# Kernel tuning notes

Hardware: AMD Instinct MI355X
Metric: run time of the kernel (lower is better)

The kernel has to match this reference:

```python
import jax, jax.numpy as jnp
import numpy as np

B, L, SD, PD, H, HD, OH = 2, 256, 64, 32, 4, 16, 32
EXP = 64  # MBConv hidden = pair_dim * expand_ratio(2)
SE = 16   # squeezed channels = int(64 * 0.25)


def _ln(x, g, b, eps=1e-5):
    m = jnp.mean(x, -1, keepdims=True)
    v = jnp.mean((x - m) ** 2, -1, keepdims=True)
    return (x - m) / jnp.sqrt(v + eps) * g + b


def _inorm(x, eps=1e-5):  # InstanceNorm2d (no affine), x: [B,C,H,W]
    m = jnp.mean(x, (2, 3), keepdims=True)
    v = jnp.mean((x - m) ** 2, (2, 3), keepdims=True)
    return (x - m) / jnp.sqrt(v + eps)


def setup_inputs() -> dict:
    key = jax.random.key(0)
    ks = jax.random.split(key, 16)
    s = jnp.float32(0.02)
    return dict(
        seq_repr=jax.random.normal(ks[0], (B, L, SD), jnp.float32),
        pair_repr=jax.random.normal(ks[1], (B, L, L, PD), jnp.float32),
        g_attn=jnp.ones((SD,), jnp.float32), b_attn=jnp.zeros((SD,), jnp.float32),
        g_pair=jnp.ones((PD,), jnp.float32), b_pair=jnp.zeros((PD,), jnp.float32),
        W_opm_lin=jax.random.normal(ks[2], (SD, OH), jnp.float32) * s,
        b_opm_lin=jnp.zeros((OH,), jnp.float32),
        g_opm=jnp.ones((OH * OH,), jnp.float32), b_opm=jnp.zeros((OH * OH,), jnp.float32),
        W_opm_proj=jax.random.normal(ks[3], (OH * OH, PD), jnp.float32) * s,
        b_opm_proj=jnp.zeros((PD,), jnp.float32),
        W_exp=jax.random.normal(ks[4], (EXP, PD), jnp.float32) * s,
        W_dw=jax.random.normal(ks[5], (EXP, 1, 3, 3), jnp.float32) * s,
        W_se1=jax.random.normal(ks[6], (SE, EXP), jnp.float32) * s,
        b_se1=jnp.zeros((SE,), jnp.float32),
        W_se2=jax.random.normal(ks[7], (EXP, SE), jnp.float32) * s,
        b_se2=jnp.zeros((EXP,), jnp.float32),
        W_pw=jax.random.normal(ks[8], (PD, EXP), jnp.float32) * s,
        W_qkv=jax.random.normal(ks[9], (SD, 3 * SD), jnp.float32) * s,
        W_outp=jax.random.normal(ks[10], (SD, SD), jnp.float32) * s,
        b_outp=jnp.zeros((SD,), jnp.float32),
        W_bias=jax.random.normal(ks[11], (PD, H), jnp.float32) * s,
    )


def reference(seq_repr, pair_repr, g_attn, b_attn, g_pair, b_pair,
              W_opm_lin, b_opm_lin, g_opm, b_opm, W_opm_proj, b_opm_proj,
              W_exp, W_dw, W_se1, b_se1, W_se2, b_se2, W_pw,
              W_qkv, W_outp, b_outp, W_bias):
    # --- OuterProductMean on attn_norm(seq) ---
    x = _ln(seq_repr, g_attn, b_attn)                            # [B,L,SD]
    a = x @ W_opm_lin + b_opm_lin                                # [B,L,OH]
    outer = jnp.einsum('bid,bje->bijde', a, a).reshape(B, L, L, OH * OH)
    op = _ln(outer, g_opm, b_opm) @ W_opm_proj + b_opm_proj      # [B,L,L,PD]
    pair = pair_repr + op
    # --- MBConv pair processor on pair_norm(pair) ---
    pn = _ln(pair, g_pair, b_pair)
    z0 = jnp.transpose(pn, (0, 3, 1, 2))                         # NCHW [B,PD,L,L]
    h = jax.nn.silu(_inorm(jnp.einsum('bcij,oc->boij', z0, W_exp)))
    h = jax.lax.conv_general_dilated(h, W_dw, (1, 1), 'SAME',
                                     feature_group_count=EXP,
                                     dimension_numbers=('NCHW', 'OIHW', 'NCHW'))
    h = jax.nn.silu(_inorm(h))
    sq = jnp.mean(h, (2, 3), keepdims=True)                      # squeeze [B,EXP,1,1]
    sq = jax.nn.silu(jnp.einsum('bcij,oc->boij', sq, W_se1) + b_se1[None, :, None, None])
    sq = jax.nn.sigmoid(jnp.einsum('bcij,oc->boij', sq, W_se2) + b_se2[None, :, None, None])
    h = h * sq
    h = _inorm(jnp.einsum('bcij,oc->boij', h, W_pw))             # project back to PD
    pair = pair + jnp.transpose(z0 + h, (0, 2, 3, 1))            # MBConv residual + outer residual
    # --- Pairwise-bias attention ---
    pn2 = _ln(pair, g_pair, b_pair)
    bias = jnp.einsum('bijp,ph->bhij', pn2, W_bias)              # [B,H,L,L]
    q, k, v = jnp.split(x @ W_qkv, 3, axis=-1)
    q = q.reshape(B, L, H, HD).transpose(0, 2, 1, 3)
    k = k.reshape(B, L, H, HD).transpose(0, 2, 1, 3)
    v = v.reshape(B, L, H, HD).transpose(0, 2, 1, 3)
    scores = jnp.einsum('bhid,bhjd->bhij', q, k) / jnp.sqrt(jnp.float32(HD)) + bias
    w = jax.nn.softmax(scores, axis=-1)
    ctx = jnp.einsum('bhij,bhjd->bhid', w, v).transpose(0, 2, 1, 3).reshape(B, L, SD)
    seq = seq_repr + ctx @ W_outp + b_outp
    return seq, pair
```

## Files before the change

kernel.cpp:

```cpp
#include <hip/hip_runtime.h>
#include <hip/hip_bf16.h>

#define LLSZ 65536
#define INV_LL (1.f / 65536.f)


__device__ __forceinline__ void chan_stats(const float* sum, const float* sumsq,
                                           int chan, float& m, float& isd)
{
    m = sum[chan] * INV_LL;
    float var = sumsq[chan] * INV_LL - m * m;
    isd = rsqrtf(var + 1e-5f);
}

__device__ __forceinline__ float silu(float t) { return t / (1.f + expf(-t)); }

__global__ __launch_bounds__(256) void kA(
    const float* __restrict__ g_opm, const float* __restrict__ b_opm,
    const float* __restrict__ Wproj, const float* __restrict__ b_proj,
    float* __restrict__ G, float* __restrict__ GW, float* __restrict__ BW,
    float* __restrict__ stats0,
    const float* __restrict__ seq, const float* __restrict__ g_attn,
    const float* __restrict__ b_attn, const float* __restrict__ W_lin,
    const float* __restrict__ b_lin, const float* __restrict__ W_qkv,
    float* __restrict__ a, float* __restrict__ am, float* __restrict__ s2,
    float* __restrict__ qkv)
{
    int tid = threadIdx.x;
    if (blockIdx.x == 0) {
        for (int k = tid; k < 768; k += 256) stats0[k] = 0.f;
        int p = tid & 31, rg = tid >> 5;
        float gw = 0.f, bw = 0.f;
        #pragma unroll 8
        for (int k = 0; k < 128; ++k) {
            int de = k * 8 + rg;
            float wv = Wproj[de * 32 + p];
            float gv = g_opm[de] * wv;
            G[de * 32 + p] = gv;
            gw += gv;
            bw += b_opm[de] * wv;
        }
        __shared__ float rG[256], rB[256];
        rG[rg * 32 + p] = gw;
        rB[rg * 32 + p] = bw;
        __syncthreads();
        for (int s = 4; s > 0; s >>= 1) {
            if (rg < s) {
                rG[rg * 32 + p] += rG[(rg + s) * 32 + p];
                rB[rg * 32 + p] += rB[(rg + s) * 32 + p];
            }
            __syncthreads();
        }
        if (tid < 32) { GW[p] = rG[p]; BW[p] = rB[p] + b_proj[p]; }
    } else {
        __shared__ float Wq[64 * 192];
        __shared__ float Wl[64 * 32];
        __shared__ float xL[4][64];
        #pragma unroll
        for (int k = 0; k < 48; ++k) Wq[k * 256 + tid] = W_qkv[k * 256 + tid];
        #pragma unroll
        for (int k = 0; k < 8; ++k) Wl[k * 256 + tid] = W_lin[k * 256 + tid];
        int sub = tid >> 6, t = tid & 63;
        int row = (blockIdx.x - 1) * 4 + sub;
        float v = seq[row * 64 + t];
        float m = v;
        for (int k = 32; k > 0; k >>= 1) m += __shfl_xor(m, k, 64);
        m *= (1.f / 64.f);
        float d = v - m;
        float var = d * d;
        for (int k = 32; k > 0; k >>= 1) var += __shfl_xor(var, k, 64);
        var *= (1.f / 64.f);
        float x = d * rsqrtf(var + 1e-5f) * g_attn[t] + b_attn[t];
        xL[sub][t] = x;
        __syncthreads();
        if (t < 32) {
            float s = 0.f;
            #pragma unroll
            for (int dd = 0; dd < 64; ++dd) s += xL[sub][dd] * Wl[dd * 32 + t];
            s += b_lin[t];
            a[row * 32 + t] = s;
            float mm = s, ss = s * s;
            for (int k = 16; k > 0; k >>= 1) {
                mm += __shfl_xor(mm, k, 32);
                ss += __shfl_xor(ss, k, 32);
            }
            if (t == 0) { am[row] = mm * (1.f / 32.f); s2[row] = ss * (1.f / 32.f); }
        }
        #pragma unroll
        for (int c3 = 0; c3 < 3; ++c3) {
            int c = c3 * 64 + t;
            float s = 0.f;
            #pragma unroll
            for (int dd = 0; dd < 64; ++dd) s += xL[sub][dd] * Wq[dd * 192 + c];
            qkv[row * 192 + c] = s;
        }
    }
}

__global__ __launch_bounds__(256) void k2_T(
    const float* __restrict__ a, const float* __restrict__ G, float* __restrict__ T)
{
    int row = blockIdx.x;
    int tid = threadIdx.x;
    __shared__ float aL[32];
    if (tid < 32) aL[tid] = a[row * 32 + tid];
    __syncthreads();
    for (int k = 0; k < 4; ++k) {
        int idx = k * 256 + tid;
        float s = 0.f;
        #pragma unroll
        for (int d = 0; d < 32; ++d) s += aL[d] * G[d * 1024 + idx];
        T[row * 1024 + idx] = s;
    }
}

__global__ __launch_bounds__(256) void k3_op(
    const float* __restrict__ a, const float* __restrict__ am,
    const float* __restrict__ s2, const float* __restrict__ T,
    const float* __restrict__ GW, const float* __restrict__ BW,
    const float* __restrict__ pair_in, float* __restrict__ pair1)
{
    int blk = blockIdx.x;
    int row = blk >> 3;
    int jg = blk & 7;
    int b = row >> 8;
    int j0 = jg * 32;
    int tid = threadIdx.x;
    __shared__ float Tl[1024];
    __shared__ float aL[32 * 33];
    __shared__ float amL[32], s2L[32], gwL[32], bwL[32];
    ((float4*)Tl)[tid] = ((const float4*)(T + (long)row * 1024))[tid];
    for (int k = 0; k < 4; ++k) {
        int idx = k * 256 + tid;
        aL[(idx >> 5) * 33 + (idx & 31)] = a[(b * 256 + j0) * 32 + idx];
    }
    if (tid < 32) {
        amL[tid] = am[b * 256 + j0 + tid];
        s2L[tid] = s2[b * 256 + j0 + tid];
        gwL[tid] = GW[tid];
        bwL[tid] = BW[tid];
    }
    __syncthreads();
    int jl = tid >> 3, cq = tid & 7;
    float am_i = am[row], s2_i = s2[row];
    float m = am_i * amL[jl];
    float isd = rsqrtf(s2_i * s2L[jl] - m * m + 1e-5f);
    long base = ((long)row * 256 + j0 + jl) * 32 + cq * 4;
    float4 pv = *(const float4*)(pair_in + base);
    float o[4];
    #pragma unroll
    for (int u = 0; u < 4; ++u) {
        int p = cq * 4 + u;
        float S = 0.f;
        #pragma unroll
        for (int e = 0; e < 32; ++e) S += aL[jl * 33 + e] * Tl[e * 32 + p];
        o[u] = isd * (S - m * gwL[p]) + bwL[p];
    }
    pv.x += o[0]; pv.y += o[1]; pv.z += o[2]; pv.w += o[3];
    *(float4*)(pair1 + base) = pv;
}

__global__ __launch_bounds__(256) void k4_expand(
    const float* __restrict__ pair1, const float* __restrict__ g_pair,
    const float* __restrict__ b_pair, const float* __restrict__ W_exp,
    float* __restrict__ e1)
{
    int b = blockIdx.x >> 9;
    int oh = (blockIdx.x >> 8) & 1;
    int px = (blockIdx.x & 255) * 256 + threadIdx.x;
    long pixel = (long)b * LLSZ + px;
    float x[32];
    const float4* src = (const float4*)(pair1 + pixel * 32);
    #pragma unroll
    for (int k = 0; k < 8; ++k) {
        float4 v = src[k];
        x[k * 4 + 0] = v.x; x[k * 4 + 1] = v.y;
        x[k * 4 + 2] = v.z; x[k * 4 + 3] = v.w;
    }
    float s = 0.f, q = 0.f;
    #pragma unroll
    for (int c = 0; c < 32; ++c) { s += x[c]; q += x[c] * x[c]; }
    float mu = s * (1.f / 32.f);
    float isd = rsqrtf(q * (1.f / 32.f) - mu * mu + 1e-5f);
    #pragma unroll
    for (int c = 0; c < 32; ++c)
        x[c] = (x[c] - mu) * isd * g_pair[c] + b_pair[c];
    float* dst = e1 + ((long)(b * 64 + oh * 32)) * LLSZ + px;
    #pragma unroll
    for (int oo = 0; oo < 32; ++oo) {
        int o = oh * 32 + oo;
        float acc = 0.f;
        #pragma unroll
        for (int c = 0; c < 32; ++c) acc += x[c] * W_exp[o * 32 + c];
        dst[(long)oo * LLSZ] = acc;
    }
}

__global__ __launch_bounds__(256) void k_stats(
    const float* __restrict__ buf, float* __restrict__ sum, float* __restrict__ sumsq)
{
    int bid = blockIdx.x;
    int chan = bid >> 3, seg = bid & 7;
    int tid = threadIdx.x;
    const float4* p = (const float4*)(buf + (long)chan * LLSZ + seg * 8192);
    float s = 0.f, ss = 0.f;
    #pragma unroll
    for (int k = 0; k < 8; ++k) {
        float4 v = p[k * 256 + tid];
        s += v.x + v.y + v.z + v.w;
        ss += v.x * v.x + v.y * v.y + v.z * v.z + v.w * v.w;
    }
    for (int k = 32; k > 0; k >>= 1) { s += __shfl_xor(s, k, 64); ss += __shfl_xor(ss, k, 64); }
    __shared__ float rs[4], rq[4];
    int wave = tid >> 6;
    if ((tid & 63) == 0) { rs[wave] = s; rq[wave] = ss; }
    __syncthreads();
    if (tid == 0) {
        atomicAdd(&sum[chan], rs[0] + rs[1] + rs[2] + rs[3]);
        atomicAdd(&sumsq[chan], rq[0] + rq[1] + rq[2] + rq[3]);
    }
}

__global__ __launch_bounds__(256) void k6_dw(
    const float* __restrict__ e1, const float* __restrict__ st1s,
    const float* __restrict__ st1q, const float* __restrict__ W_dw,
    float* __restrict__ h2, float* __restrict__ st2s, float* __restrict__ st2q)
{
    int blk = blockIdx.x;
    int chan = blk >> 5;
    int r0 = (blk & 31) * 8;
    int o = chan & 63;
    int tid = threadIdx.x;
    float m, isd;
    chan_stats(st1s, st1q, chan, m, isd);
    __shared__ float sL[10][258];
    const float* src = e1 + (long)chan * LLSZ;
    for (int k = tid; k < 640; k += 256) {
        int rr = k >> 6, c4 = k & 63;
        int g = r0 - 1 + rr;
        float4 v = make_float4(0.f, 0.f, 0.f, 0.f);
        bool ok = (g >= 0 && g < 256);
        if (ok) v = *(const float4*)(src + g * 256 + c4 * 4);
        float t;
        t = (v.x - m) * isd; v.x = ok ? silu(t) : 0.f;
        t = (v.y - m) * isd; v.y = ok ? silu(t) : 0.f;
        t = (v.z - m) * isd; v.z = ok ? silu(t) : 0.f;
        t = (v.w - m) * isd; v.w = ok ? silu(t) : 0.f;
        sL[rr][1 + c4 * 4 + 0] = v.x;
        sL[rr][1 + c4 * 4 + 1] = v.y;
        sL[rr][1 + c4 * 4 + 2] = v.z;
        sL[rr][1 + c4 * 4 + 3] = v.w;
    }
    if (tid < 10) { sL[tid][0] = 0.f; sL[tid][257] = 0.f; }
    float w[9];
    #pragma unroll
    for (int k = 0; k < 9; ++k) w[k] = W_dw[o * 9 + k];
    __syncthreads();
    int c = tid;
    float bs = 0.f, bq = 0.f;
    #pragma unroll
    for (int rr = 0; rr < 8; ++rr) {
        float s = 0.f;
        #pragma unroll
        for (int ki = 0; ki < 3; ++ki)
            #pragma unroll
            for (int kj = 0; kj < 3; ++kj)
                s += sL[rr + ki][c + kj] * w[ki * 3 + kj];
        h2[(long)chan * LLSZ + (r0 + rr) * 256 + c] = s;
        bs += s; bq += s * s;
    }
    for (int k = 32; k > 0; k >>= 1) { bs += __shfl_xor(bs, k, 64); bq += __shfl_xor(bq, k, 64); }
    __shared__ float r2s[4], r2q[4];
    int wave = tid >> 6;
    if ((tid & 63) == 0) { r2s[wave] = bs; r2q[wave] = bq; }
    __syncthreads();
    if (tid == 0) {
        atomicAdd(&st2s[chan], r2s[0] + r2s[1] + r2s[2] + r2s[3]);
        atomicAdd(&st2q[chan], r2q[0] + r2q[1] + r2q[2] + r2q[3]);
    }
}

__global__ __launch_bounds__(256) void k8_squeeze(
    const float* __restrict__ h2, const float* __restrict__ st2s,
    const float* __restrict__ st2q, float* __restrict__ sqs)
{
    int bid = blockIdx.x;
    int chan = bid >> 3, seg = bid & 7;
    int tid = threadIdx.x;
    float m, isd;
    chan_stats(st2s, st2q, chan, m, isd);
    const float4* p = (const float4*)(h2 + (long)chan * LLSZ + seg * 8192);
    float s = 0.f;
    #pragma unroll
    for (int k = 0; k < 8; ++k) {
        float4 v = p[k * 256 + tid];
        s += silu((v.x - m) * isd) + silu((v.y - m) * isd)
           + silu((v.z - m) * isd) + silu((v.w - m) * isd);
    }
    for (int k = 32; k > 0; k >>= 1) s += __shfl_xor(s, k, 64);
    __shared__ float rs[4];
    int wave = tid >> 6;
    if ((tid & 63) == 0) rs[wave] = s;
    __syncthreads();
    if (tid == 0) atomicAdd(&sqs[chan], rs[0] + rs[1] + rs[2] + rs[3]);
}

__global__ __launch_bounds__(256) void k10_pw(
    const float* __restrict__ h2, const float* __restrict__ st2s,
    const float* __restrict__ st2q, const float* __restrict__ sqs,
    const float* __restrict__ W_se1, const float* __restrict__ b_se1,
    const float* __restrict__ W_se2, const float* __restrict__ b_se2,
    const float* __restrict__ W_pw, float* __restrict__ hp)
{
    int b = blockIdx.x >> 8;
    int px = (blockIdx.x & 255) * 256 + threadIdx.x;
    int tid = threadIdx.x;
    __shared__ float s1L[16];
    __shared__ float sqvL[64];
    if (tid < 16) {
        float s = 0.f;
        for (int c = 0; c < 64; ++c) s += sqs[b * 64 + c] * W_se1[tid * 64 + c];
        s = s * INV_LL + b_se1[tid];
        s1L[tid] = silu(s);
    }
    __syncthreads();
    if (tid < 64) {
        float s = 0.f;
        #pragma unroll
        for (int j = 0; j < 16; ++j) s += s1L[j] * W_se2[tid * 16 + j];
        s += b_se2[tid];
        sqvL[tid] = 1.f / (1.f + expf(-s));
    }
    __syncthreads();
    float v[64];
    const float* src = h2 + ((long)b * 64) * LLSZ + px;
    #pragma unroll
    for (int c = 0; c < 64; ++c) v[c] = src[(long)c * LLSZ];
    __builtin_amdgcn_sched_barrier(0);
    float acc[32];
    #pragma unroll
    for (int p = 0; p < 32; ++p) acc[p] = 0.f;
    #pragma unroll
    for (int c = 0; c < 64; ++c) {
        float m, isd;
        chan_stats(st2s, st2q, b * 64 + c, m, isd);
        float x = silu((v[c] - m) * isd) * sqvL[c];
        #pragma unroll
        for (int p = 0; p < 32; ++p) acc[p] += x * W_pw[p * 64 + c];
    }
    float* dst = hp + ((long)b * 32) * LLSZ + px;
    #pragma unroll
    for (int p = 0; p < 32; ++p) dst[(long)p * LLSZ] = acc[p];
}

__global__ __launch_bounds__(256) void k12_merge(
    const float* __restrict__ pair1, const float* __restrict__ hp,
    const float* __restrict__ st3s, const float* __restrict__ st3q,
    const float* __restrict__ g_pair, const float* __restrict__ b_pair,
    const float* __restrict__ W_bias, float* __restrict__ pair_out,
    float* __restrict__ biasbuf)
{
    int b = blockIdx.x >> 8;
    int px = (blockIdx.x & 255) * 256 + threadIdx.x;
    long pixel = (long)b * LLSZ + px;
    float4 r[8];
    const float4* src = (const float4*)(pair1 + pixel * 32);
    #pragma unroll
    for (int k = 0; k < 8; ++k) r[k] = src[k];
    float hv[32];
    const float* hpb = hp + ((long)b * 32) * LLSZ + px;
    #pragma unroll
    for (int p = 0; p < 32; ++p) hv[p] = hpb[(long)p * LLSZ];
    __builtin_amdgcn_sched_barrier(0);
    float v1[32];
    #pragma unroll
    for (int k = 0; k < 8; ++k) {
        v1[k * 4 + 0] = r[k].x; v1[k * 4 + 1] = r[k].y;
        v1[k * 4 + 2] = r[k].z; v1[k * 4 + 3] = r[k].w;
    }
    float s = 0.f, q = 0.f;
    #pragma unroll
    for (int c = 0; c < 32; ++c) { s += v1[c]; q += v1[c] * v1[c]; }
    float mu = s * (1.f / 32.f);
    float isd = rsqrtf(q * (1.f / 32.f) - mu * mu + 1e-5f);
    float vo[32];
    #pragma unroll
    for (int p = 0; p < 32; ++p) {
        float m3, isd3;
        chan_stats(st3s, st3q, b * 32 + p, m3, isd3);
        float pnv = (v1[p] - mu) * isd * g_pair[p] + b_pair[p];
        vo[p] = v1[p] + pnv + (hv[p] - m3) * isd3;
    }
    float4* dst = (float4*)(pair_out + pixel * 32);
    #pragma unroll
    for (int k = 0; k < 8; ++k)
        dst[k] = make_float4(vo[k * 4], vo[k * 4 + 1], vo[k * 4 + 2], vo[k * 4 + 3]);
    float s2_ = 0.f, q2 = 0.f;
    #pragma unroll
    for (int c = 0; c < 32; ++c) { s2_ += vo[c]; q2 += vo[c] * vo[c]; }
    float mu2 = s2_ * (1.f / 32.f);
    float isd2 = rsqrtf(q2 * (1.f / 32.f) - mu2 * mu2 + 1e-5f);
    float t[4] = {0.f, 0.f, 0.f, 0.f};
    #pragma unroll
    for (int p = 0; p < 32; ++p) {
        float pn2 = (vo[p] - mu2) * isd2 * g_pair[p] + b_pair[p];
        #pragma unroll
        for (int h = 0; h < 4; ++h) t[h] += pn2 * W_bias[p * 4 + h];
    }
    #pragma unroll
    for (int h = 0; h < 4; ++h)
        biasbuf[((long)(b * 4 + h)) * LLSZ + px] = t[h];
}

__global__ __launch_bounds__(256) void k13_attn(
    const float* __restrict__ qkv, const float* __restrict__ biasbuf,
    float* __restrict__ ctx)
{
    int blk = blockIdx.x;
    int b = blk >> 8;
    int h = (blk >> 6) & 3;
    int ig = blk & 63;
    int tid = threadIdx.x;
    int wave = tid >> 6, lane = tid & 63;
    __shared__ float kL[16][256];
    __shared__ float vL[16][256];
    {
        const float4* kr = (const float4*)(qkv + ((long)(b * 256 + tid)) * 192 + 64 + h * 16);
        float4 k0 = kr[0], k1 = kr[1], k2 = kr[2], k3 = kr[3];
        const float4* vr = (const float4*)(qkv + ((long)(b * 256 + tid)) * 192 + 128 + h * 16);
        float4 w0 = vr[0], w1 = vr[1], w2 = vr[2], w3 = vr[3];
        kL[ 0][tid] = k0.x; kL[ 1][tid] = k0.y; kL[ 2][tid] = k0.z; kL[ 3][tid] = k0.w;
        kL[ 4][tid] = k1.x; kL[ 5][tid] = k1.y; kL[ 6][tid] = k1.z; kL[ 7][tid] = k1.w;
        kL[ 8][tid] = k2.x; kL[ 9][tid] = k2.y; kL[10][tid] = k2.z; kL[11][tid] = k2.w;
        kL[12][tid] = k3.x; kL[13][tid] = k3.y; kL[14][tid] = k3.z; kL[15][tid] = k3.w;
        vL[ 0][tid] = w0.x; vL[ 1][tid] = w0.y; vL[ 2][tid] = w0.z; vL[ 3][tid] = w0.w;
        vL[ 4][tid] = w1.x; vL[ 5][tid] = w1.y; vL[ 6][tid] = w1.z; vL[ 7][tid] = w1.w;
        vL[ 8][tid] = w2.x; vL[ 9][tid] = w2.y; vL[10][tid] = w2.z; vL[11][tid] = w2.w;
        vL[12][tid] = w3.x; vL[13][tid] = w3.y; vL[14][tid] = w3.z; vL[15][tid] = w3.w;
    }
    __syncthreads();
    int i = ig * 4 + wave;
    const float* qrow = qkv + ((long)(b * 256 + i)) * 192 + h * 16;
    float qv[16];
    #pragma unroll
    for (int d = 0; d < 16; ++d) qv[d] = qrow[d];
    float sj[4];
    #pragma unroll
    for (int q = 0; q < 4; ++q) {
        int j = 64 * q + lane;
        float s = 0.f;
        #pragma unroll
        for (int d = 0; d < 16; ++d) s += qv[d] * kL[d][j];
        sj[q] = s * 0.25f + biasbuf[((long)(b * 4 + h)) * LLSZ + i * 256 + j];
    }
    float mx = fmaxf(fmaxf(sj[0], sj[1]), fmaxf(sj[2], sj[3]));
    for (int k = 32; k > 0; k >>= 1) mx = fmaxf(mx, __shfl_xor(mx, k, 64));
    float wgt[4], wsum = 0.f;
    #pragma unroll
    for (int q = 0; q < 4; ++q) { wgt[q] = expf(sj[q] - mx); wsum += wgt[q]; }
    for (int k = 32; k > 0; k >>= 1) wsum += __shfl_xor(wsum, k, 64);
    float inv = 1.f / wsum;
    float o[16];
    #pragma unroll
    for (int d = 0; d < 16; ++d) o[d] = 0.f;
    #pragma unroll
    for (int q = 0; q < 4; ++q) {
        int j = 64 * q + lane;
        #pragma unroll
        for (int d = 0; d < 16; ++d) o[d] += wgt[q] * vL[d][j];
    }
    #pragma unroll
    for (int d = 0; d < 16; ++d)
        for (int k = 32; k > 0; k >>= 1) o[d] += __shfl_xor(o[d], k, 64);
    if (lane == 0) {
        #pragma unroll
        for (int d = 0; d < 16; ++d)
            ctx[((long)(b * 256 + i)) * 64 + h * 16 + d] = o[d] * inv;
    }
}

__global__ __launch_bounds__(256) void k14_seqout(
    const float* __restrict__ seq, const float* __restrict__ ctx,
    const float* __restrict__ W_outp, const float* __restrict__ b_outp,
    float* __restrict__ out)
{
    __shared__ float Wo[64 * 64];
    __shared__ float cL[4][64];
    int tid = threadIdx.x;
    #pragma unroll
    for (int k = 0; k < 16; ++k) Wo[k * 256 + tid] = W_outp[k * 256 + tid];
    int sub = tid >> 6, t = tid & 63;
    int row = blockIdx.x * 4 + sub;
    cL[sub][t] = ctx[row * 64 + t];
    __syncthreads();
    float s = b_outp[t];
    #pragma unroll
    for (int u = 0; u < 64; ++u) s += cL[sub][u] * Wo[u * 64 + t];
    out[row * 64 + t] = seq[row * 64 + t] + s;
}

extern "C" void kernel_launch(void* const* d_in, const int* in_sizes, int n_in,
                              void* d_out, int out_size, void* d_ws, size_t ws_size,
                              hipStream_t stream) {
    const float* seq_repr   = (const float*)d_in[0];
    const float* pair_repr  = (const float*)d_in[1];
    const float* g_attn     = (const float*)d_in[2];
    const float* b_attn     = (const float*)d_in[3];
    const float* g_pair     = (const float*)d_in[4];
    const float* b_pair     = (const float*)d_in[5];
    const float* W_opm_lin  = (const float*)d_in[6];
    const float* b_opm_lin  = (const float*)d_in[7];
    const float* g_opm      = (const float*)d_in[8];
    const float* b_opm      = (const float*)d_in[9];
    const float* W_opm_proj = (const float*)d_in[10];
    const float* b_opm_proj = (const float*)d_in[11];
    const float* W_exp      = (const float*)d_in[12];
    const float* W_dw       = (const float*)d_in[13];
    const float* W_se1      = (const float*)d_in[14];
    const float* b_se1      = (const float*)d_in[15];
    const float* W_se2      = (const float*)d_in[16];
    const float* b_se2      = (const float*)d_in[17];
    const float* W_pw       = (const float*)d_in[18];
    const float* W_qkv      = (const float*)d_in[19];
    const float* W_outp     = (const float*)d_in[20];
    const float* b_outp     = (const float*)d_in[21];
    const float* W_bias     = (const float*)d_in[22];

    float* out_seq  = (float*)d_out;
    float* out_pair = (float*)d_out + 32768;

    float* w = (float*)d_ws;
    float* a_buf   = w;
    float* am_buf  = a_buf + 16384;
    float* s2_buf  = am_buf + 512;
    float* qkv_buf = s2_buf + 512;
    float* G_buf   = qkv_buf + 98304;
    float* GW_buf  = G_buf + 32768;
    float* BW_buf  = GW_buf + 32;
    float* ctx     = BW_buf + 32;
    float* st1s    = ctx + 32768;
    float* st1q    = st1s + 128;
    float* st2s    = st1q + 128;
    float* st2q    = st2s + 128;
    float* st3s    = st2q + 128;
    float* st3q    = st3s + 64;
    float* sqs     = st3q + 64;
    float* T_buf   = sqs + 128;
    float* biasb   = T_buf;
    float* pair1   = T_buf + 524288;
    float* e1      = pair1 + 4194304;
    float* hp      = e1;
    float* h2      = e1 + 8388608;

    hipLaunchKernelGGL(kA, dim3(129), dim3(256), 0, stream,
                       g_opm, b_opm, W_opm_proj, b_opm_proj, G_buf, GW_buf, BW_buf,
                       st1s,
                       seq_repr, g_attn, b_attn, W_opm_lin, b_opm_lin, W_qkv,
                       a_buf, am_buf, s2_buf, qkv_buf);
    hipLaunchKernelGGL(k2_T, dim3(512), dim3(256), 0, stream, a_buf, G_buf, T_buf);
    hipLaunchKernelGGL(k3_op, dim3(4096), dim3(256), 0, stream,
                       a_buf, am_buf, s2_buf, T_buf, GW_buf, BW_buf,
                       pair_repr, pair1);
    hipLaunchKernelGGL(k4_expand, dim3(1024), dim3(256), 0, stream,
                       pair1, g_pair, b_pair, W_exp, e1);
    hipLaunchKernelGGL(k_stats, dim3(1024), dim3(256), 0, stream, e1, st1s, st1q);
    hipLaunchKernelGGL(k6_dw, dim3(4096), dim3(256), 0, stream,
                       e1, st1s, st1q, W_dw, h2, st2s, st2q);
    hipLaunchKernelGGL(k8_squeeze, dim3(1024), dim3(256), 0, stream,
                       h2, st2s, st2q, sqs);
    hipLaunchKernelGGL(k10_pw, dim3(512), dim3(256), 0, stream,
                       h2, st2s, st2q, sqs, W_se1, b_se1, W_se2, b_se2,
                       W_pw, hp);
    hipLaunchKernelGGL(k_stats, dim3(512), dim3(256), 0, stream, hp, st3s, st3q);
    hipLaunchKernelGGL(k12_merge, dim3(512), dim3(256), 0, stream,
                       pair1, hp, st3s, st3q, g_pair, b_pair, W_bias,
                       out_pair, biasb);
    hipLaunchKernelGGL(k13_attn, dim3(512), dim3(256), 0, stream,
                       qkv_buf, biasb, ctx);
    hipLaunchKernelGGL(k14_seqout, dim3(128), dim3(256), 0, stream,
                       seq_repr, ctx, W_outp, b_outp, out_seq);
}
```

Baseline: 298.8 us.

## Stage pixel tiles in shared memory and split output channels across waves

Three per-pixel kernels (expand, pointwise projection, merge) are changed from one thread per pixel holding every channel to blocks of 64 pixels staged through LDS. Global loads become coalesced float4 reads, and each wave computes a subset of output channels, or each thread a quarter of a pixel's channels combined with shuffles. This cuts register pressure, which should raise occupancy, and the grid grows from 512 or 1024 blocks to 2048. In exchange, expand and merge recompute the LayerNorm statistics redundantly per wave or lane, and the extra barriers and LDS traffic add cost.

```diff
diff --git a/kernel.cpp b/kernel.cpp
--- a/kernel.cpp
+++ b/kernel.cpp
@@ -165,18 +165,25 @@
     const float* __restrict__ b_pair, const float* __restrict__ W_exp,
     float* __restrict__ e1)
 {
-    int b = blockIdx.x >> 9;
-    int oh = (blockIdx.x >> 8) & 1;
-    int px = (blockIdx.x & 255) * 256 + threadIdx.x;
-    long pixel = (long)b * LLSZ + px;
+    int b = blockIdx.x >> 10;
+    int px0 = (blockIdx.x & 1023) * 64;
+    int tid = threadIdx.x;
+    __shared__ float pnL[64 * 33];
+    #pragma unroll
+    for (int k = 0; k < 2; ++k) {
+        int idx = k * 256 + tid;
+        int px = idx >> 3, cq = idx & 7;
+        float4 v = *(const float4*)(pair1 + ((long)b * LLSZ + px0 + px) * 32 + cq * 4);
+        pnL[px * 33 + cq * 4 + 0] = v.x;
+        pnL[px * 33 + cq * 4 + 1] = v.y;
+        pnL[px * 33 + cq * 4 + 2] = v.z;
+        pnL[px * 33 + cq * 4 + 3] = v.w;
+    }
+    __syncthreads();
+    int px = tid & 63, og = tid >> 6;
     float x[32];
-    const float4* src = (const float4*)(pair1 + pixel * 32);
-    #pragma unroll
-    for (int k = 0; k < 8; ++k) {
-        float4 v = src[k];
-        x[k * 4 + 0] = v.x; x[k * 4 + 1] = v.y;
-        x[k * 4 + 2] = v.z; x[k * 4 + 3] = v.w;
-    }
+    #pragma unroll
+    for (int c = 0; c < 32; ++c) x[c] = pnL[px * 33 + c];
     float s = 0.f, q = 0.f;
     #pragma unroll
     for (int c = 0; c < 32; ++c) { s += x[c]; q += x[c] * x[c]; }
@@ -185,14 +192,14 @@
     #pragma unroll
     for (int c = 0; c < 32; ++c)
         x[c] = (x[c] - mu) * isd * g_pair[c] + b_pair[c];
-    float* dst = e1 + ((long)(b * 64 + oh * 32)) * LLSZ + px;
-    #pragma unroll
-    for (int oo = 0; oo < 32; ++oo) {
-        int o = oh * 32 + oo;
+    float* dst = e1 + ((long)(b * 64 + og * 16)) * LLSZ + px0 + px;
+    #pragma unroll
+    for (int k = 0; k < 16; ++k) {
+        int o = og * 16 + k;
         float acc = 0.f;
         #pragma unroll
         for (int c = 0; c < 32; ++c) acc += x[c] * W_exp[o * 32 + c];
-        dst[(long)oo * LLSZ] = acc;
+        dst[(long)k * LLSZ] = acc;
     }
 }
 
@@ -312,11 +319,12 @@
     const float* __restrict__ W_se2, const float* __restrict__ b_se2,
     const float* __restrict__ W_pw, float* __restrict__ hp)
 {
-    int b = blockIdx.x >> 8;
-    int px = (blockIdx.x & 255) * 256 + threadIdx.x;
+    int b = blockIdx.x >> 10;
+    int px0 = (blockIdx.x & 1023) * 64;
     int tid = threadIdx.x;
     __shared__ float s1L[16];
-    __shared__ float sqvL[64];
+    __shared__ float sqvL[64], mL[64], iL[64];
+    __shared__ float hL[64 * 64];
     if (tid < 16) {
         float s = 0.f;
         for (int c = 0; c < 64; ++c) s += sqs[b * 64 + c] * W_se1[tid * 64 + c];
@@ -330,27 +338,37 @@
         for (int j = 0; j < 16; ++j) s += s1L[j] * W_se2[tid * 16 + j];
         s += b_se2[tid];
         sqvL[tid] = 1.f / (1.f + expf(-s));
-    }
-    __syncthreads();
-    float v[64];
-    const float* src = h2 + ((long)b * 64) * LLSZ + px;
-    #pragma unroll
-    for (int c = 0; c < 64; ++c) v[c] = src[(long)c * LLSZ];
-    __builtin_amdgcn_sched_barrier(0);
-    float acc[32];
-    #pragma unroll
-    for (int p = 0; p < 32; ++p) acc[p] = 0.f;
+        float m, isd;
+        chan_stats(st2s, st2q, b * 64 + tid, m, isd);
+        mL[tid] = m; iL[tid] = isd;
+    }
+    __syncthreads();
+    #pragma unroll
+    for (int k = 0; k < 4; ++k) {
+        int idx = k * 256 + tid;
+        int c = idx >> 4, cq = idx & 15;
+        float m = mL[c], isd = iL[c], sc = sqvL[c];
+        float4 v = *(const float4*)(h2 + (long)(b * 64 + c) * LLSZ + px0 + cq * 4);
+        v.x = silu((v.x - m) * isd) * sc;
+        v.y = silu((v.y - m) * isd) * sc;
+        v.z = silu((v.z - m) * isd) * sc;
+        v.w = silu((v.w - m) * isd) * sc;
+        *(float4*)(hL + c * 64 + cq * 4) = v;
+    }
+    __syncthreads();
+    int px = tid & 63, og = tid >> 6;
+    float acc[8];
+    #pragma unroll
+    for (int u = 0; u < 8; ++u) acc[u] = 0.f;
     #pragma unroll
     for (int c = 0; c < 64; ++c) {
-        float m, isd;
-        chan_stats(st2s, st2q, b * 64 + c, m, isd);
-        float x = silu((v[c] - m) * isd) * sqvL[c];
-        #pragma unroll
-        for (int p = 0; p < 32; ++p) acc[p] += x * W_pw[p * 64 + c];
-    }
-    float* dst = hp + ((long)b * 32) * LLSZ + px;
-    #pragma unroll
-    for (int p = 0; p < 32; ++p) dst[(long)p * LLSZ] = acc[p];
+        float x = hL[c * 64 + px];
+        #pragma unroll
+        for (int u = 0; u < 8; ++u) acc[u] += x * W_pw[(og * 8 + u) * 64 + c];
+    }
+    float* dst = hp + ((long)(b * 32 + og * 8)) * LLSZ + px0 + px;
+    #pragma unroll
+    for (int u = 0; u < 8; ++u) dst[(long)u * LLSZ] = acc[u];
 }
 
 __global__ __launch_bounds__(256) void k12_merge(
@@ -360,56 +378,80 @@
     const float* __restrict__ W_bias, float* __restrict__ pair_out,
     float* __restrict__ biasbuf)
 {
-    int b = blockIdx.x >> 8;
-    int px = (blockIdx.x & 255) * 256 + threadIdx.x;
-    long pixel = (long)b * LLSZ + px;
-    float4 r[8];
-    const float4* src = (const float4*)(pair1 + pixel * 32);
-    #pragma unroll
-    for (int k = 0; k < 8; ++k) r[k] = src[k];
-    float hv[32];
-    const float* hpb = hp + ((long)b * 32) * LLSZ + px;
-    #pragma unroll
-    for (int p = 0; p < 32; ++p) hv[p] = hpb[(long)p * LLSZ];
-    __builtin_amdgcn_sched_barrier(0);
-    float v1[32];
-    #pragma unroll
-    for (int k = 0; k < 8; ++k) {
-        v1[k * 4 + 0] = r[k].x; v1[k * 4 + 1] = r[k].y;
-        v1[k * 4 + 2] = r[k].z; v1[k * 4 + 3] = r[k].w;
-    }
+    int b = blockIdx.x >> 10;
+    int px0 = (blockIdx.x & 1023) * 64;
+    int tid = threadIdx.x;
+    __shared__ float pnL[64 * 33];
+    __shared__ float hpN[32 * 65];
+    #pragma unroll
+    for (int k = 0; k < 2; ++k) {
+        int idx = k * 256 + tid;
+        int px = idx >> 3, cq = idx & 7;
+        float4 v = *(const float4*)(pair1 + ((long)b * LLSZ + px0 + px) * 32 + cq * 4);
+        pnL[px * 33 + cq * 4 + 0] = v.x;
+        pnL[px * 33 + cq * 4 + 1] = v.y;
+        pnL[px * 33 + cq * 4 + 2] = v.z;
+        pnL[px * 33 + cq * 4 + 3] = v.w;
+    }
+    #pragma unroll
+    for (int k = 0; k < 2; ++k) {
+        int idx = k * 256 + tid;
+        int c = idx >> 4, cq = idx & 15;
+        float m3, isd3;
+        chan_stats(st3s, st3q, b * 32 + c, m3, isd3);
+        float4 v = *(const float4*)(hp + (long)(b * 32 + c) * LLSZ + px0 + cq * 4);
+        hpN[c * 65 + cq * 4 + 0] = (v.x - m3) * isd3;
+        hpN[c * 65 + cq * 4 + 1] = (v.y - m3) * isd3;
+        hpN[c * 65 + cq * 4 + 2] = (v.z - m3) * isd3;
+        hpN[c * 65 + cq * 4 + 3] = (v.w - m3) * isd3;
+    }
+    __syncthreads();
+    int px = tid >> 2, part = tid & 3;
+    float v1[8];
+    #pragma unroll
+    for (int u = 0; u < 8; ++u) v1[u] = pnL[px * 33 + part * 8 + u];
     float s = 0.f, q = 0.f;
     #pragma unroll
-    for (int c = 0; c < 32; ++c) { s += v1[c]; q += v1[c] * v1[c]; }
+    for (int u = 0; u < 8; ++u) { s += v1[u]; q += v1[u] * v1[u]; }
+    s += __shfl_xor(s, 1, 4); q += __shfl_xor(q, 1, 4);
+    s += __shfl_xor(s, 2, 4); q += __shfl_xor(q, 2, 4);
     float mu = s * (1.f / 32.f);
     float isd = rsqrtf(q * (1.f / 32.f) - mu * mu + 1e-5f);
-    float vo[32];
-    #pragma unroll
-    for (int p = 0; p < 32; ++p) {
-        float m3, isd3;
-        chan_stats(st3s, st3q, b * 32 + p, m3, isd3);
-        float pnv = (v1[p] - mu) * isd * g_pair[p] + b_pair[p];
-        vo[p] = v1[p] + pnv + (hv[p] - m3) * isd3;
-    }
-    float4* dst = (float4*)(pair_out + pixel * 32);
-    #pragma unroll
-    for (int k = 0; k < 8; ++k)
-        dst[k] = make_float4(vo[k * 4], vo[k * 4 + 1], vo[k * 4 + 2], vo[k * 4 + 3]);
+    float vo[8];
+    #pragma unroll
+    for (int u = 0; u < 8; ++u) {
+        int c = part * 8 + u;
+        float pnv = (v1[u] - mu) * isd * g_pair[c] + b_pair[c];
+        vo[u] = v1[u] + pnv + hpN[c * 65 + px];
+    }
+    long obase = ((long)b * LLSZ + px0 + px) * 32 + part * 8;
+    *(float4*)(pair_out + obase)     = make_float4(vo[0], vo[1], vo[2], vo[3]);
+    *(float4*)(pair_out + obase + 4) = make_float4(vo[4], vo[5], vo[6], vo[7]);
     float s2_ = 0.f, q2 = 0.f;
     #pragma unroll
-    for (int c = 0; c < 32; ++c) { s2_ += vo[c]; q2 += vo[c] * vo[c]; }
+    for (int u = 0; u < 8; ++u) { s2_ += vo[u]; q2 += vo[u] * vo[u]; }
+    s2_ += __shfl_xor(s2_, 1, 4); q2 += __shfl_xor(q2, 1, 4);
+    s2_ += __shfl_xor(s2_, 2, 4); q2 += __shfl_xor(q2, 2, 4);
     float mu2 = s2_ * (1.f / 32.f);
     float isd2 = rsqrtf(q2 * (1.f / 32.f) - mu2 * mu2 + 1e-5f);
     float t[4] = {0.f, 0.f, 0.f, 0.f};
     #pragma unroll
-    for (int p = 0; p < 32; ++p) {
-        float pn2 = (vo[p] - mu2) * isd2 * g_pair[p] + b_pair[p];
-        #pragma unroll
-        for (int h = 0; h < 4; ++h) t[h] += pn2 * W_bias[p * 4 + h];
-    }
-    #pragma unroll
-    for (int h = 0; h < 4; ++h)
-        biasbuf[((long)(b * 4 + h)) * LLSZ + px] = t[h];
+    for (int u = 0; u < 8; ++u) {
+        int c = part * 8 + u;
+        float pn2 = (vo[u] - mu2) * isd2 * g_pair[c] + b_pair[c];
+        #pragma unroll
+        for (int h = 0; h < 4; ++h) t[h] += pn2 * W_bias[c * 4 + h];
+    }
+    #pragma unroll
+    for (int h = 0; h < 4; ++h) {
+        t[h] += __shfl_xor(t[h], 1, 4);
+        t[h] += __shfl_xor(t[h], 2, 4);
+    }
+    if (part == 0) {
+        #pragma unroll
+        for (int h = 0; h < 4; ++h)
+            biasbuf[((long)(b * 4 + h)) * LLSZ + px0 + px] = t[h];
+    }
 }
 
 __global__ __launch_bounds__(256) void k13_attn(
@@ -561,18 +603,18 @@
     hipLaunchKernelGGL(k3_op, dim3(4096), dim3(256), 0, stream,
                        a_buf, am_buf, s2_buf, T_buf, GW_buf, BW_buf,
                        pair_repr, pair1);
-    hipLaunchKernelGGL(k4_expand, dim3(1024), dim3(256), 0, stream,
+    hipLaunchKernelGGL(k4_expand, dim3(2048), dim3(256), 0, stream,
                        pair1, g_pair, b_pair, W_exp, e1);
     hipLaunchKernelGGL(k_stats, dim3(1024), dim3(256), 0, stream, e1, st1s, st1q);
     hipLaunchKernelGGL(k6_dw, dim3(4096), dim3(256), 0, stream,
                        e1, st1s, st1q, W_dw, h2, st2s, st2q);
     hipLaunchKernelGGL(k8_squeeze, dim3(1024), dim3(256), 0, stream,
                        h2, st2s, st2q, sqs);
-    hipLaunchKernelGGL(k10_pw, dim3(512), dim3(256), 0, stream,
+    hipLaunchKernelGGL(k10_pw, dim3(2048), dim3(256), 0, stream,
                        h2, st2s, st2q, sqs, W_se1, b_se1, W_se2, b_se2,
                        W_pw, hp);
     hipLaunchKernelGGL(k_stats, dim3(512), dim3(256), 0, stream, hp, st3s, st3q);
-    hipLaunchKernelGGL(k12_merge, dim3(512), dim3(256), 0, stream,
+    hipLaunchKernelGGL(k12_merge, dim3(2048), dim3(256), 0, stream,
                        pair1, hp, st3s, st3q, g_pair, b_pair, W_bias,
                        out_pair, biasb);
     hipLaunchKernelGGL(k13_attn, dim3(512), dim3(256), 0, stream,
```

After: 299.2 us. Within noise of the previous version (+0.1%).
